# Kernel tuning notes

Measured on AMD Instinct MI355X. Metric: run time of the kernel, lower is better.

## Reference

```python
import jax, jax.numpy as jnp
import numpy as np

BLOCK = 32  # 2**basic_block

def _hadamard(n):
    H = np.array([[1.0]], dtype=np.float32)
    while H.shape[0] < n:
        H = np.block([[H, H], [H, -H]])
    return H


def setup_inputs() -> dict:
    key = jax.random.key(0)
    ks = jax.random.split(key, 9)
    B, T, I, Hd, O = 64, 512, 128, 1024, 128
    sgn = lambda k, shp: jnp.where(jax.random.normal(k, shp) >= 0, 1.0, -1.0).astype(jnp.float32)
    return {
        "x": jax.random.normal(ks[0], (B, T, I), dtype=jnp.float32),
        "W_in": jax.random.normal(ks[1], (I, Hd), dtype=jnp.float32) / np.sqrt(I),
        "s1": sgn(ks[2], (Hd,)),                      # Binadamard sign vector (layer 1)
        "b1": 0.01 * jax.random.normal(ks[3], (Hd,), dtype=jnp.float32),
        "s2": sgn(ks[4], (Hd,)),                      # Binadamard sign vector (layer 2, full)
        "b2": 0.01 * jax.random.normal(ks[5], (Hd,), dtype=jnp.float32),
        "Wbn": sgn(ks[6], (Hd, Hd)) / np.sqrt(Hd),    # BinaryNorm: sign(W)/sqrt(n), materialized
        "W_out": jax.random.normal(ks[7], (Hd, O), dtype=jnp.float32) / np.sqrt(Hd),
        "b_out": jax.random.normal(ks[8], (O,), dtype=jnp.float32),
    }


def reference(x, W_in, s1, b1, s2, b2, Wbn, W_out, b_out):
    B, T, _ = x.shape
    Hd = s1.shape[0]
    Hb = jnp.asarray(_hadamard(BLOCK) / np.sqrt(BLOCK), dtype=x.dtype)   # [32,32]
    Hf = jnp.asarray(_hadamard(Hd) / np.sqrt(Hd), dtype=x.dtype)         # [Hd,Hd]
    u = jnp.einsum('bti,ih->tbh', x, W_in)  # precompute input projections, time-major

    def step(carry, u_t):
        h1, h2 = carry
        # layer 1: block-diagonal sign*Hadamard recurrence + input
        h1 = s1 * (h1.reshape(B, -1, BLOCK) @ Hb).reshape(B, Hd) + b1 + u_t
        h1b = jax.nn.relu(h1)
        # layer 2: full sign*Hadamard recurrence + binary-norm projection of h1b
        h2 = s2 * (h2 @ Hf) + b2 + h1b @ Wbn
        return (h1, h2), None

    h0 = jnp.zeros((B, Hd), dtype=x.dtype)
    (_, h2), _ = jax.lax.scan(step, (h0, h0), u)
    h2b = jax.nn.relu(h2)
    return h2b @ W_out + b_out
```

## Files before the change

### kernel.cpp

```cpp
#include <hip/hip_runtime.h>

#define B_ 64
#define T_ 512
#define I_ 128
#define H_ 1024
#define O_ 128

typedef unsigned short u16;
typedef unsigned int u32;
typedef __attribute__((ext_vector_type(8))) short short8v;
typedef __attribute__((ext_vector_type(4))) float float4v;

typedef __attribute__((address_space(1))) const void gvoid_t;
typedef __attribute__((address_space(3))) void svoid_t;

__device__ __forceinline__ u16 f2bf(float f) {
  union { float f; u32 u; } v; v.f = f;
  u32 r = v.u + 0x7FFF + ((v.u >> 16) & 1);
  return (u16)(r >> 16);
}
__device__ __forceinline__ float bf2f(u16 b) {
  union { u32 u; float f; } v; v.u = ((u32)b) << 16;
  return v.f;
}
__device__ __forceinline__ float bits2f(u32 b) {
  union { u32 u; float f; } v; v.u = b;
  return v.f;
}

__device__ __forceinline__ float fwht32(float x, int lane) {
#pragma unroll
  for (int s = 1; s <= 16; s <<= 1) {
    const float y = __shfl_xor(x, s);
    x = (lane & s) ? (y - x) : (x + y);
  }
  return x;
}

__device__ __forceinline__ void fwht32_reg(float* x) {
#pragma unroll
  for (int s = 1; s < 32; s <<= 1)
#pragma unroll
    for (int i = 0; i < 32; ++i)
      if (!(i & s)) { const float a = x[i], b = x[i | s]; x[i] = a + b; x[i | s] = a - b; }
}

__device__ __forceinline__ void transpose32(float* x, float (*T)[33], int t) {
#pragma unroll
  for (int c = 0; c < 32; ++c) T[t][c] = x[c];
#pragma unroll
  for (int c = 0; c < 32; ++c) x[c] = T[c][t];
}

__global__ __launch_bounds__(256) void prep_all(const float* __restrict__ x, const float* __restrict__ Wbn,
                                                const float* __restrict__ W_in, u16* __restrict__ xT,
                                                u16* __restrict__ WbnT, u16* __restrict__ WinT) {
  __shared__ float tl[32][33];
  const int blk = blockIdx.x;
  const int tid = threadIdx.x;
  if (blk < 1024) {
    const int bx = blk & 31, by = blk >> 5;
    const int c = tid & 31, r8 = tid >> 5;
#pragma unroll
    for (int i = 0; i < 4; ++i) {
      const int r = r8 + i * 8;
      tl[r][c] = Wbn[(size_t)(by * 32 + r) * 1024 + bx * 32 + c];
    }
    __syncthreads();
#pragma unroll
    for (int i = 0; i < 4; ++i) {
      const int r = r8 + i * 8;
      WbnT[(size_t)(bx * 32 + r) * 1024 + by * 32 + c] = f2bf(tl[c][r]);
    }
  } else if (blk < 1152) {
    const int t2 = blk - 1024;
    const int bx = t2 & 31, by = t2 >> 5;
    const int c = tid & 31, r8 = tid >> 5;
#pragma unroll
    for (int i = 0; i < 4; ++i) {
      const int r = r8 + i * 8;
      tl[r][c] = W_in[(size_t)(by * 32 + r) * 1024 + bx * 32 + c];
    }
    __syncthreads();
#pragma unroll
    for (int i = 0; i < 4; ++i) {
      const int r = r8 + i * 8;
      WinT[(size_t)(bx * 32 + r) * 128 + by * 32 + c] = f2bf(tl[c][r]);
    }
  } else {
    const int idx = (blk - 1152) * 256 + tid;
    const int i = idx & (I_ - 1);
    const int r = idx >> 7;
    const int b = r & (B_ - 1);
    const int t = r >> 6;
    xT[idx] = f2bf(x[((size_t)b * T_ + t) * I_ + i]);
  }
}

template <int K, bool BIAS>
__global__ __launch_bounds__(256) void gemm_bf16(const u16* __restrict__ A, const u16* __restrict__ Bt,
                                                 u16* __restrict__ C, const float* __restrict__ bias) {
  __shared__ u16 As[128 * 64];
  __shared__ u16 Bs[128 * 64];
  const int tid = threadIdx.x;
  const int bm = blockIdx.x, bn = blockIdx.y;
  const int lane = tid & 63, w = tid >> 6;
  const int wr = w >> 1, wc = w & 1;
  const int l16 = lane & 15, lq = lane >> 4;

  float4v acc[4][4];
#pragma unroll
  for (int mi = 0; mi < 4; ++mi)
#pragma unroll
    for (int ni = 0; ni < 4; ++ni)
#pragma unroll
      for (int j = 0; j < 4; ++j) acc[mi][ni][j] = 0.f;

  const int srow = w * 32 + (lane >> 3);
  const int scol = (((lane & 7) ^ (lane >> 3)) << 3);
  const u16* Ag = A + (size_t)(bm * 128 + srow) * K + scol;
  const u16* Bg = Bt + (size_t)(bn * 128 + srow) * K + scol;

  for (int k0 = 0; k0 < K; k0 += 64) {
    __syncthreads();
#pragma unroll
    for (int i = 0; i < 4; ++i) {
      __builtin_amdgcn_global_load_lds((gvoid_t*)(Ag + k0 + (size_t)i * 8 * K),
                                       (svoid_t*)&As[(w * 32 + i * 8) * 64], 16, 0, 0);
      __builtin_amdgcn_global_load_lds((gvoid_t*)(Bg + k0 + (size_t)i * 8 * K),
                                       (svoid_t*)&Bs[(w * 32 + i * 8) * 64], 16, 0, 0);
    }
    __syncthreads();
#pragma unroll
    for (int ks = 0; ks < 2; ++ks) {
      short8v a[4], bf[4];
#pragma unroll
      for (int mi = 0; mi < 4; ++mi) {
        const int row = wr * 64 + mi * 16 + l16;
        a[mi] = *(const short8v*)&As[row * 64 + (((ks * 4 + lq) ^ (row & 7)) << 3)];
      }
#pragma unroll
      for (int ni = 0; ni < 4; ++ni) {
        const int row = wc * 64 + ni * 16 + l16;
        bf[ni] = *(const short8v*)&Bs[row * 64 + (((ks * 4 + lq) ^ (row & 7)) << 3)];
      }
#pragma unroll
      for (int mi = 0; mi < 4; ++mi)
#pragma unroll
        for (int ni = 0; ni < 4; ++ni)
          acc[mi][ni] = __builtin_amdgcn_mfma_f32_16x16x32_bf16(a[mi], bf[ni], acc[mi][ni], 0, 0, 0);
    }
  }

#pragma unroll
  for (int mi = 0; mi < 4; ++mi)
#pragma unroll
    for (int ni = 0; ni < 4; ++ni) {
      const int row = bm * 128 + wr * 64 + mi * 16 + lq * 4;
      const int col = bn * 128 + wc * 64 + ni * 16 + l16;
      const float bv = BIAS ? bias[col] : 0.f;
#pragma unroll
      for (int j = 0; j < 4; ++j) C[(size_t)(row + j) * H_ + col] = f2bf(acc[mi][ni][j] + bv);
    }
}

__global__ __launch_bounds__(1024) void h1_Pinit(const float* __restrict__ s1, float* __restrict__ P) {
  const int hb = blockIdx.x;
  const int tid = threadIdx.x;
  const int j = tid >> 5, r = tid & 31;
  const int lane = tid & 63;
  const float sc = s1[hb * 32 + r] * 0.17677669529663687f;
  float x = (r == j) ? 1.f : 0.f;
  for (int it = 0; it < 16; ++it) x = sc * fwht32(x, lane);
  P[(size_t)hb * 1024 + r * 32 + j] = x;
}

__global__ __launch_bounds__(64) void h1_local(const u16* __restrict__ u, const float* __restrict__ s1,
                                               float* __restrict__ Ybuf) {
  const int g = blockIdx.x * 64 + threadIdx.x;
  const int hb = g & 31, b = (g >> 5) & 63, chunk = g >> 11;
  float x[32], sc[32];
#pragma unroll
  for (int i = 0; i < 32; i += 4) {
    const float4 s4 = *(const float4*)&s1[hb * 32 + i];
    sc[i] = s4.x * 0.17677669529663687f;
    sc[i + 1] = s4.y * 0.17677669529663687f;
    sc[i + 2] = s4.z * 0.17677669529663687f;
    sc[i + 3] = s4.w * 0.17677669529663687f;
  }
#pragma unroll
  for (int i = 0; i < 32; ++i) x[i] = 0.f;
  const u16* up = u + ((size_t)(chunk * 16) * B_ + b) * H_ + hb * 32;
#pragma unroll 2
  for (int k = 0; k < 16; ++k) {
    u32 wv[16];
#pragma unroll
    for (int j = 0; j < 4; ++j) {
      const uint4 t4 = *(const uint4*)(up + (size_t)k * (B_ * H_) + j * 8);
      wv[4 * j] = t4.x; wv[4 * j + 1] = t4.y; wv[4 * j + 2] = t4.z; wv[4 * j + 3] = t4.w;
    }
    fwht32_reg(x);
#pragma unroll
    for (int i2 = 0; i2 < 16; ++i2) {
      x[2 * i2]     = fmaf(sc[2 * i2],     x[2 * i2],     bits2f(wv[i2] << 16));
      x[2 * i2 + 1] = fmaf(sc[2 * i2 + 1], x[2 * i2 + 1], bits2f(wv[i2] & 0xFFFF0000u));
    }
  }
  float* yp = Ybuf + (size_t)g * 32;
#pragma unroll
  for (int i = 0; i < 32; i += 4) {
    float4 o; o.x = x[i]; o.y = x[i + 1]; o.z = x[i + 2]; o.w = x[i + 3];
    *(float4*)(yp + i) = o;
  }
}

__global__ __launch_bounds__(64) void h1_carry(const float* __restrict__ P, const float* __restrict__ Ybuf,
                                               float* __restrict__ Zbuf) {
  const int hpair = blockIdx.x, b = blockIdx.y;
  const int lane = threadIdx.x;
  const int r = lane & 31, hb = hpair * 2 + (lane >> 5);
  const float* Prow = P + (size_t)hb * 1024 + r * 32;
  float pr[32];
#pragma unroll
  for (int j = 0; j < 32; ++j) pr[j] = Prow[j];
  float z = 0.f;
  const int base = lane & 32;
  for (int c = 0; c < 32; ++c) {
    Zbuf[(((size_t)c * 64 + b) * 32 + hb) * 32 + r] = z;
    if (c < 31) {
      const float yv = Ybuf[(((size_t)c * 64 + b) * 32 + hb) * 32 + r];
      float zn = 0.f;
#pragma unroll
      for (int j = 0; j < 32; ++j) zn = fmaf(pr[j], __shfl(z, base + j), zn);
      z = zn + yv;
    }
  }
}

__global__ __launch_bounds__(64) void h1_apply(u16* __restrict__ u, const float* __restrict__ s1,
                                               const float* __restrict__ Zbuf) {
  const int g = blockIdx.x * 64 + threadIdx.x;
  const int hb = g & 31, b = (g >> 5) & 63, chunk = g >> 11;
  float x[32], sc[32];
#pragma unroll
  for (int i = 0; i < 32; i += 4) {
    const float4 s4 = *(const float4*)&s1[hb * 32 + i];
    sc[i] = s4.x * 0.17677669529663687f;
    sc[i + 1] = s4.y * 0.17677669529663687f;
    sc[i + 2] = s4.z * 0.17677669529663687f;
    sc[i + 3] = s4.w * 0.17677669529663687f;
  }
  const float* zp = Zbuf + (size_t)g * 32;
#pragma unroll
  for (int i = 0; i < 32; i += 4) {
    const float4 z4 = *(const float4*)(zp + i);
    x[i] = z4.x; x[i + 1] = z4.y; x[i + 2] = z4.z; x[i + 3] = z4.w;
  }
  u16* up = u + ((size_t)(chunk * 16) * B_ + b) * H_ + hb * 32;
#pragma unroll 2
  for (int k = 0; k < 16; ++k) {
    u32 wv[16];
#pragma unroll
    for (int j = 0; j < 4; ++j) {
      const uint4 t4 = *(const uint4*)(up + (size_t)k * (B_ * H_) + j * 8);
      wv[4 * j] = t4.x; wv[4 * j + 1] = t4.y; wv[4 * j + 2] = t4.z; wv[4 * j + 3] = t4.w;
    }
    fwht32_reg(x);
#pragma unroll
    for (int i2 = 0; i2 < 16; ++i2) {
      x[2 * i2]     = fmaf(sc[2 * i2],     x[2 * i2],     bits2f(wv[i2] << 16));
      x[2 * i2 + 1] = fmaf(sc[2 * i2 + 1], x[2 * i2 + 1], bits2f(wv[i2] & 0xFFFF0000u));
    }
    u32 ov[16];
#pragma unroll
    for (int i2 = 0; i2 < 16; ++i2) {
      const u32 lo = f2bf(fmaxf(x[2 * i2], 0.f));
      const u32 hi = f2bf(fmaxf(x[2 * i2 + 1], 0.f));
      ov[i2] = lo | (hi << 16);
    }
#pragma unroll
    for (int j = 0; j < 4; ++j) {
      uint4 t4; t4.x = ov[4 * j]; t4.y = ov[4 * j + 1]; t4.z = ov[4 * j + 2]; t4.w = ov[4 * j + 3];
      *(uint4*)(up + (size_t)k * (B_ * H_) + j * 8) = t4;
    }
  }
}

__global__ __launch_bounds__(256) void fwht_chunk(const u16* __restrict__ V, const float* __restrict__ s2,
                                                  u16* __restrict__ A32, u16* __restrict__ Y) {
  __shared__ float tr[4][2][32][33];
  const int wv = threadIdx.x >> 6;
  const int lane = threadIdx.x & 63;
  const int slot = lane >> 5, t = lane & 31;
  float (*T)[33] = tr[wv][slot];
  const int gs = blockIdx.x * 8 + wv * 2 + slot;

  float x[32], s0[32], s1[32];
#pragma unroll
  for (int c = 0; c < 32; ++c) {
    s0[c] = s2[t * 32 + c] * 0.03125f;
    s1[c] = s2[c * 32 + t] * 0.03125f;
  }

  if (gs < 1024) {
    const int W = gs;
#pragma unroll
    for (int c = 0; c < 32; ++c) x[c] = (t * 32 + c == W) ? 1.f : 0.f;
    for (int j = 0; j < 32; ++j) {
      if (j & 1) {
#pragma unroll
        for (int c = 0; c < 32; ++c) x[c] *= s1[c];
      } else {
#pragma unroll
        for (int c = 0; c < 32; ++c) x[c] *= s0[c];
      }
      fwht32_reg(x);
      transpose32(x, T, t);
      fwht32_reg(x);
    }
    u16* dst = A32 + (size_t)W * H_ + t * 32;
    u32 ov[16];
#pragma unroll
    for (int c = 0; c < 16; ++c) ov[c] = (u32)f2bf(x[2 * c]) | ((u32)f2bf(x[2 * c + 1]) << 16);
#pragma unroll
    for (int j = 0; j < 4; ++j) {
      uint4 t4; t4.x = ov[4 * j]; t4.y = ov[4 * j + 1]; t4.z = ov[4 * j + 2]; t4.w = ov[4 * j + 3];
      *(uint4*)(dst + j * 8) = t4;
    }
  } else {
    const int s = gs - 1024;
    const int c0 = s >> 6, b = s & 63;
    const u16* Vbase = V + ((size_t)(c0 * 32) * B_ + b) * H_;
#pragma unroll
    for (int c = 0; c < 32; ++c) x[c] = 0.f;
    for (int j = 0; j < 32; ++j) {
      const u16* vrow = Vbase + (size_t)j * (B_ * H_);
      const int pe = (j + 1) & 1;
      u32 vpk[16];
      u16 vsc[32];
      if (pe == 0) {
#pragma unroll
        for (int q = 0; q < 4; ++q) {
          const uint4 t4 = *(const uint4*)(vrow + t * 32 + q * 8);
          vpk[4 * q] = t4.x; vpk[4 * q + 1] = t4.y; vpk[4 * q + 2] = t4.z; vpk[4 * q + 3] = t4.w;
        }
      } else {
#pragma unroll
        for (int c = 0; c < 32; ++c) vsc[c] = vrow[c * 32 + t];
      }
      fwht32_reg(x);
      transpose32(x, T, t);
      fwht32_reg(x);
      if (pe == 0) {
#pragma unroll
        for (int c = 0; c < 16; ++c) {
          x[2 * c]     = fmaf(s0[2 * c],     x[2 * c],     bits2f(vpk[c] << 16));
          x[2 * c + 1] = fmaf(s0[2 * c + 1], x[2 * c + 1], bits2f(vpk[c] & 0xFFFF0000u));
        }
      } else {
#pragma unroll
        for (int c = 0; c < 32; ++c) x[c] = fmaf(s1[c], x[c], bf2f(vsc[c]));
      }
    }
    u16* dst = Y + ((size_t)c0 * B_ + b) * H_ + t * 32;
    u32 ov[16];
#pragma unroll
    for (int c = 0; c < 16; ++c) ov[c] = (u32)f2bf(x[2 * c]) | ((u32)f2bf(x[2 * c + 1]) << 16);
#pragma unroll
    for (int j = 0; j < 4; ++j) {
      uint4 t4; t4.x = ov[4 * j]; t4.y = ov[4 * j + 1]; t4.z = ov[4 * j + 2]; t4.w = ov[4 * j + 3];
      *(uint4*)(dst + j * 8) = t4;
    }
  }
}

template <bool FIRST, bool LAST>
__global__ __launch_bounds__(256) void combine(const u16* __restrict__ Zold, const u16* __restrict__ Yc,
                                               const u16* __restrict__ A32, u16* __restrict__ Znew,
                                               float* __restrict__ h2out) {
  const int rt = blockIdx.x >> 6, nt = blockIdx.x & 63;
  const int tid = threadIdx.x;
  __shared__ float red[4][16][16];
  if (!FIRST) {
    const int w = tid >> 6, lane = tid & 63, l16 = lane & 15, lq = lane >> 4;
    float4v acc = {0.f, 0.f, 0.f, 0.f};
    const u16* Ap = Zold + (size_t)(rt * 16 + l16) * H_ + w * 256 + lq * 8;
    const u16* Bp = A32 + (size_t)(nt * 16 + l16) * H_ + w * 256 + lq * 8;
#pragma unroll
    for (int ks = 0; ks < 8; ++ks) {
      short8v a = *(const short8v*)(Ap + ks * 32);
      short8v bb = *(const short8v*)(Bp + ks * 32);
      acc = __builtin_amdgcn_mfma_f32_16x16x32_bf16(a, bb, acc, 0, 0, 0);
    }
#pragma unroll
    for (int j = 0; j < 4; ++j) red[w][lq * 4 + j][l16] = acc[j];
    __syncthreads();
  } else {
    __syncthreads();
  }
  const int row = tid >> 4, col = tid & 15;
  float s = 0.f;
  if (!FIRST) s = red[0][row][col] + red[1][row][col] + red[2][row][col] + red[3][row][col];
  const int b = rt * 16 + row, n = nt * 16 + col;
  s += bf2f(Yc[(size_t)b * H_ + n]);
  if (LAST) h2out[(size_t)b * H_ + n] = s;
  else Znew[(size_t)b * H_ + n] = f2bf(s);
}

__global__ __launch_bounds__(128) void final_out(const float* __restrict__ h2, const float* __restrict__ W_out,
                                                 const float* __restrict__ b_out, float* __restrict__ out) {
  __shared__ float hrow[H_];
  const int b = blockIdx.x, o = threadIdx.x;
  for (int i = o; i < H_; i += 128) hrow[i] = fmaxf(h2[(size_t)b * H_ + i], 0.f);
  __syncthreads();
  float acc = b_out[o];
  for (int h = 0; h < H_; ++h) acc = fmaf(hrow[h], W_out[(size_t)h * O_ + o], acc);
  out[b * O_ + o] = acc;
}

extern "C" void kernel_launch(void* const* d_in, const int* in_sizes, int n_in,
                              void* d_out, int out_size, void* d_ws, size_t ws_size,
                              hipStream_t stream) {
  const float* x     = (const float*)d_in[0];
  const float* W_in  = (const float*)d_in[1];
  const float* s1    = (const float*)d_in[2];
  const float* b1    = (const float*)d_in[3];
  const float* s2    = (const float*)d_in[4];
  const float* b2    = (const float*)d_in[5];
  const float* Wbn   = (const float*)d_in[6];
  const float* W_out = (const float*)d_in[7];
  const float* b_out = (const float*)d_in[8];
  float* out = (float*)d_out;

  char* ws = (char*)d_ws;
  u16* u      = (u16*)ws;
  u16* V      = (u16*)(ws + 67108864);
  float* P1   = (float*)(ws + 67108864);
  float* Zbuf = (float*)(ws + 69206016);
  u16* xT     = (u16*)(ws + 134217728);
  float* Ybuf = (float*)(ws + 134217728);
  u16* WbnT   = (u16*)(ws + 142606336);
  u16* WinT   = (u16*)(ws + 144703488);
  u16* A32    = (u16*)(ws + 134217728);
  u16* Y      = (u16*)(ws + 136314880);
  u16* Zb0    = (u16*)(ws + 138412032);
  u16* Zb1    = (u16*)(ws + 138543104);
  float* h2   = (float*)(ws + 138674176);

  prep_all<<<17536, 256, 0, stream>>>(x, Wbn, W_in, xT, WbnT, WinT);
  h1_Pinit<<<32, 1024, 0, stream>>>(s1, P1);
  gemm_bf16<128, true><<<dim3(256, 8), 256, 0, stream>>>(xT, WinT, u, b1);
  h1_local<<<1024, 64, 0, stream>>>(u, s1, Ybuf);
  h1_carry<<<dim3(16, 64), 64, 0, stream>>>(P1, Ybuf, Zbuf);
  h1_apply<<<1024, 64, 0, stream>>>(u, s1, Zbuf);
  gemm_bf16<1024, true><<<dim3(256, 8), 256, 0, stream>>>(u, WbnT, V, b2);
  fwht_chunk<<<256, 256, 0, stream>>>(V, s2, A32, Y);

  u16* Zb[2] = {Zb0, Zb1};
  combine<true, false><<<256, 256, 0, stream>>>(nullptr, Y, A32, Zb[0], nullptr);
  for (int c = 1; c < 15; ++c)
    combine<false, false><<<256, 256, 0, stream>>>(Zb[(c + 1) & 1], Y + (size_t)c * B_ * H_, A32,
                                                   Zb[c & 1], nullptr);
  combine<false, true><<<256, 256, 0, stream>>>(Zb[0], Y + (size_t)15 * B_ * H_, A32, nullptr, h2);

  final_out<<<64, 128, 0, stream>>>(h2, W_out, b_out, out);
}
```

Before: 323.6 us.

## Precompute A32 powers to combine four chunks per launch, cutting serial combines

Adds a GEMM kernel that builds the second, third and fourth powers of the 32-step transition matrix (A^64, A^96, A^128) and stores them side by side in a 4096-wide buffer. The 16 sequential combine launches become 4 launches, each folding three or four chunk contributions through those powers at once. This shortens the serial chain of small launches at the cost of two extra 1024x1024 GEMMs and an extra rounding of the matrix powers to bf16. Workspace offsets are rearranged to hold the larger buffer.

```diff
diff --git a/kernel.cpp b/kernel.cpp
--- a/kernel.cpp
+++ b/kernel.cpp
@@ -164,6 +164,74 @@
     }
 }
 
+__global__ __launch_bounds__(256) void gemm_pw(u16* __restrict__ Bt4, int stage) {
+  int xo, yo, co;
+  if (stage == 0)            { xo = 3072; yo = 3072; co = 2048; }
+  else if (blockIdx.z == 0)  { xo = 3072; yo = 2048; co = 1024; }
+  else                       { xo = 2048; yo = 2048; co = 0;    }
+  __shared__ u16 As[128][40];
+  __shared__ u16 Bs[128][40];
+  const int tid = threadIdx.x;
+  const int bn = blockIdx.x, bm = blockIdx.y;
+  const int lane = tid & 63, w = tid >> 6;
+  const int wr = w >> 1, wc = w & 1;
+  const int l16 = lane & 15, lq = lane >> 4;
+
+  float4v acc[4][4];
+#pragma unroll
+  for (int mi = 0; mi < 4; ++mi)
+#pragma unroll
+    for (int ni = 0; ni < 4; ++ni)
+#pragma unroll
+      for (int j = 0; j < 4; ++j) acc[mi][ni][j] = 0.f;
+
+  const int sr = tid >> 1;
+  const int sc = (tid & 1) << 4;
+  const u16* Ag = Bt4 + xo + (size_t)(bm * 128 + sr) * 4096 + sc;
+  const int kr = tid >> 4;
+  const int no = (tid & 15) * 8;
+
+  for (int k0 = 0; k0 < 1024; k0 += 32) {
+    uint4 a0 = *(const uint4*)(Ag + k0);
+    uint4 a1 = *(const uint4*)(Ag + k0 + 8);
+    uint4 b0 = *(const uint4*)(Bt4 + yo + (size_t)(k0 + kr) * 4096 + bn * 128 + no);
+    uint4 b1 = *(const uint4*)(Bt4 + yo + (size_t)(k0 + 16 + kr) * 4096 + bn * 128 + no);
+    __syncthreads();
+    *(uint4*)&As[sr][sc] = a0;
+    *(uint4*)&As[sr][sc + 8] = a1;
+    {
+      u16 tmp[8];
+      *(uint4*)tmp = b0;
+#pragma unroll
+      for (int i = 0; i < 8; ++i) Bs[no + i][kr] = tmp[i];
+      *(uint4*)tmp = b1;
+#pragma unroll
+      for (int i = 0; i < 8; ++i) Bs[no + i][16 + kr] = tmp[i];
+    }
+    __syncthreads();
+    short8v a[4], bf[4];
+#pragma unroll
+    for (int mi = 0; mi < 4; ++mi) a[mi] = *(const short8v*)&As[wr * 64 + mi * 16 + l16][lq * 8];
+#pragma unroll
+    for (int ni = 0; ni < 4; ++ni) bf[ni] = *(const short8v*)&Bs[wc * 64 + ni * 16 + l16][lq * 8];
+#pragma unroll
+    for (int mi = 0; mi < 4; ++mi)
+#pragma unroll
+      for (int ni = 0; ni < 4; ++ni)
+        acc[mi][ni] = __builtin_amdgcn_mfma_f32_16x16x32_bf16(a[mi], bf[ni], acc[mi][ni], 0, 0, 0);
+  }
+
+#pragma unroll
+  for (int mi = 0; mi < 4; ++mi)
+#pragma unroll
+    for (int ni = 0; ni < 4; ++ni) {
+      const int row = bm * 128 + wr * 64 + mi * 16 + lq * 4;
+      const int col = bn * 128 + wc * 64 + ni * 16 + l16;
+#pragma unroll
+      for (int j = 0; j < 4; ++j) Bt4[co + (size_t)(row + j) * 4096 + col] = f2bf(acc[mi][ni][j]);
+    }
+}
+
 __global__ __launch_bounds__(1024) void h1_Pinit(const float* __restrict__ s1, float* __restrict__ P) {
   const int hb = blockIdx.x;
   const int tid = threadIdx.x;
@@ -287,7 +355,7 @@
 }
 
 __global__ __launch_bounds__(256) void fwht_chunk(const u16* __restrict__ V, const float* __restrict__ s2,
-                                                  u16* __restrict__ A32, u16* __restrict__ Y) {
+                                                  u16* __restrict__ Bt4, u16* __restrict__ Y) {
   __shared__ float tr[4][2][32][33];
   const int wv = threadIdx.x >> 6;
   const int lane = threadIdx.x & 63;
@@ -318,7 +386,7 @@
       transpose32(x, T, t);
       fwht32_reg(x);
     }
-    u16* dst = A32 + (size_t)W * H_ + t * 32;
+    u16* dst = Bt4 + (size_t)W * 4096 + 3072 + t * 32;
     u32 ov[16];
 #pragma unroll
     for (int c = 0; c < 16; ++c) ov[c] = (u32)f2bf(x[2 * c]) | ((u32)f2bf(x[2 * c + 1]) << 16);
@@ -374,37 +442,35 @@
   }
 }
 
-template <bool FIRST, bool LAST>
-__global__ __launch_bounds__(256) void combine(const u16* __restrict__ Zold, const u16* __restrict__ Yc,
-                                               const u16* __restrict__ A32, u16* __restrict__ Znew,
-                                               float* __restrict__ h2out) {
+template <int NSEG, bool LAST>
+__global__ __launch_bounds__(256) void combine4(const u16* __restrict__ sg0, const u16* __restrict__ sg1,
+                                                const u16* __restrict__ sg2, const u16* __restrict__ sg3,
+                                                const u16* __restrict__ Yadd, const u16* __restrict__ Bt4,
+                                                u16* __restrict__ Znew, float* __restrict__ h2out) {
   const int rt = blockIdx.x >> 6, nt = blockIdx.x & 63;
   const int tid = threadIdx.x;
   __shared__ float red[4][16][16];
-  if (!FIRST) {
-    const int w = tid >> 6, lane = tid & 63, l16 = lane & 15, lq = lane >> 4;
-    float4v acc = {0.f, 0.f, 0.f, 0.f};
-    const u16* Ap = Zold + (size_t)(rt * 16 + l16) * H_ + w * 256 + lq * 8;
-    const u16* Bp = A32 + (size_t)(nt * 16 + l16) * H_ + w * 256 + lq * 8;
-#pragma unroll
-    for (int ks = 0; ks < 8; ++ks) {
+  const int w = tid >> 6, lane = tid & 63, l16 = lane & 15, lq = lane >> 4;
+  float4v acc = {0.f, 0.f, 0.f, 0.f};
+  if (w < NSEG) {
+    const u16* seg = (w == 0) ? sg0 : (w == 1) ? sg1 : (w == 2) ? sg2 : sg3;
+    const u16* Ap = seg + (size_t)(rt * 16 + l16) * H_ + lq * 8;
+    const u16* Bp = Bt4 + (size_t)(nt * 16 + l16) * 4096 + (4 - NSEG + w) * 1024 + lq * 8;
+#pragma unroll 8
+    for (int ks = 0; ks < 32; ++ks) {
       short8v a = *(const short8v*)(Ap + ks * 32);
       short8v bb = *(const short8v*)(Bp + ks * 32);
       acc = __builtin_amdgcn_mfma_f32_16x16x32_bf16(a, bb, acc, 0, 0, 0);
     }
-#pragma unroll
-    for (int j = 0; j < 4; ++j) red[w][lq * 4 + j][l16] = acc[j];
-    __syncthreads();
-  } else {
-    __syncthreads();
-  }
+  }
+#pragma unroll
+  for (int j = 0; j < 4; ++j) red[w][lq * 4 + j][l16] = acc[j];
+  __syncthreads();
   const int row = tid >> 4, col = tid & 15;
-  float s = 0.f;
-  if (!FIRST) s = red[0][row][col] + red[1][row][col] + red[2][row][col] + red[3][row][col];
-  const int b = rt * 16 + row, n = nt * 16 + col;
-  s += bf2f(Yc[(size_t)b * H_ + n]);
-  if (LAST) h2out[(size_t)b * H_ + n] = s;
-  else Znew[(size_t)b * H_ + n] = f2bf(s);
+  float s = red[0][row][col] + red[1][row][col] + red[2][row][col] + red[3][row][col];
+  s += bf2f(Yadd[(size_t)(rt * 16 + row) * H_ + nt * 16 + col]);
+  if (LAST) h2out[(size_t)(rt * 16 + row) * H_ + nt * 16 + col] = s;
+  else Znew[(size_t)(rt * 16 + row) * H_ + nt * 16 + col] = f2bf(s);
 }
 
 __global__ __launch_bounds__(128) void final_out(const float* __restrict__ h2, const float* __restrict__ W_out,
@@ -439,13 +505,13 @@
   float* Zbuf = (float*)(ws + 69206016);
   u16* xT     = (u16*)(ws + 134217728);
   float* Ybuf = (float*)(ws + 134217728);
+  u16* Bt4    = (u16*)(ws + 134217728);
   u16* WbnT   = (u16*)(ws + 142606336);
+  u16* Y      = (u16*)(ws + 142606336);
   u16* WinT   = (u16*)(ws + 144703488);
-  u16* A32    = (u16*)(ws + 134217728);
-  u16* Y      = (u16*)(ws + 136314880);
-  u16* Zb0    = (u16*)(ws + 138412032);
-  u16* Zb1    = (u16*)(ws + 138543104);
-  float* h2   = (float*)(ws + 138674176);
+  u16* Zb0    = (u16*)(ws + 144703488);
+  u16* Zb1    = (u16*)(ws + 144834560);
+  float* h2   = (float*)(ws + 144965632);
 
   prep_all<<<17536, 256, 0, stream>>>(x, Wbn, W_in, xT, WbnT, WinT);
   h1_Pinit<<<32, 1024, 0, stream>>>(s1, P1);
@@ -454,14 +520,15 @@
   h1_carry<<<dim3(16, 64), 64, 0, stream>>>(P1, Ybuf, Zbuf);
   h1_apply<<<1024, 64, 0, stream>>>(u, s1, Zbuf);
   gemm_bf16<1024, true><<<dim3(256, 8), 256, 0, stream>>>(u, WbnT, V, b2);
-  fwht_chunk<<<256, 256, 0, stream>>>(V, s2, A32, Y);
-
-  u16* Zb[2] = {Zb0, Zb1};
-  combine<true, false><<<256, 256, 0, stream>>>(nullptr, Y, A32, Zb[0], nullptr);
-  for (int c = 1; c < 15; ++c)
-    combine<false, false><<<256, 256, 0, stream>>>(Zb[(c + 1) & 1], Y + (size_t)c * B_ * H_, A32,
-                                                   Zb[c & 1], nullptr);
-  combine<false, true><<<256, 256, 0, stream>>>(Zb[0], Y + (size_t)15 * B_ * H_, A32, nullptr, h2);
+  fwht_chunk<<<256, 256, 0, stream>>>(V, s2, Bt4, Y);
+  gemm_pw<<<dim3(8, 8, 1), 256, 0, stream>>>(Bt4, 0);
+  gemm_pw<<<dim3(8, 8, 2), 256, 0, stream>>>(Bt4, 1);
+
+  const size_t BH = (size_t)B_ * H_;
+  combine4<3, false><<<256, 256, 0, stream>>>(Y, Y + BH, Y + 2 * BH, nullptr, Y + 3 * BH, Bt4, Zb0, nullptr);
+  combine4<4, false><<<256, 256, 0, stream>>>(Zb0, Y + 4 * BH, Y + 5 * BH, Y + 6 * BH, Y + 7 * BH, Bt4, Zb1, nullptr);
+  combine4<4, false><<<256, 256, 0, stream>>>(Zb1, Y + 8 * BH, Y + 9 * BH, Y + 10 * BH, Y + 11 * BH, Bt4, Zb0, nullptr);
+  combine4<4, true><<<256, 256, 0, stream>>>(Zb0, Y + 12 * BH, Y + 13 * BH, Y + 14 * BH, Y + 15 * BH, Bt4, nullptr, h2);
 
   final_out<<<64, 128, 0, stream>>>(h2, W_out, b_out, out);
 }
```

Measured after the change: 400.9 us. 1.24x slower.
